# Optimization experiments

Hardware: AMD Instinct MI355X
Metric: run time of the kernel (lower is better)

Reference implementation:

```python
import jax, jax.numpy as jnp
import numpy as np

NUM_NODES = 100000
NUM_RELS = 200
DIM = 128
NUM_EDGES = 600000


def setup_inputs() -> dict:
    key = jax.random.key(0)
    ks = jax.random.split(key, 12)
    xav = lambda k, shp: jax.random.uniform(k, shp, jnp.float32, -1.0, 1.0) * jnp.sqrt(6.0 / (shp[0] + shp[1]))
    return {
        'edge_index': jax.random.randint(ks[0], (2, NUM_EDGES), 0, NUM_NODES),
        'edge_type': jax.random.randint(ks[1], (NUM_EDGES,), 0, NUM_RELS),
        'edge_weight': jax.random.uniform(ks[2], (NUM_EDGES,), jnp.float32),
        'node_emb': xav(ks[3], (NUM_NODES, DIM)),
        'rel_emb': xav(ks[4], (NUM_RELS, DIM)),
        'W0': xav(ks[5], (DIM, DIM)),
        'Wself0': xav(ks[6], (DIM, DIM)),
        'Wrel0': xav(ks[7], (DIM, DIM)),
        'W1': xav(ks[8], (DIM, DIM)),
        'Wself1': xav(ks[9], (DIM, DIM)),
        'Wrel1': xav(ks[10], (DIM, DIM)),
    }


def comp_sub(x_src, r):
    return x_src - r


def compgcn_conv(x, rel, edge_index, edge_type, edge_weight, W, Wself, Wrel):
    src, dst = edge_index[0], edge_index[1]
    # edge-wise gather + composition: [E, D]
    msg = comp_sub(x[src], rel[edge_type])
    msg = msg * edge_weight[:, None]
    # scatter-add aggregation to destination nodes: [N, D]
    agg = jax.ops.segment_sum(msg, dst, num_segments=x.shape[0])
    x_out = agg @ W + x @ Wself
    rel_out = rel @ Wrel
    return x_out, rel_out


def reference(edge_index, edge_type, edge_weight, node_emb, rel_emb,
              W0, Wself0, Wrel0, W1, Wself1, Wrel1):
    # layer 0
    x, rel = compgcn_conv(node_emb, rel_emb, edge_index, edge_type, edge_weight,
                          W0, Wself0, Wrel0)
    # inter-layer nonlinearity (dropout is identity in eval mode)
    x = jax.nn.relu(x)
    rel = jax.nn.relu(rel)
    # layer 1 (last layer: no relu/dropout after)
    x, rel = compgcn_conv(x, rel, edge_index, edge_type, edge_weight,
                          W1, Wself1, Wrel1)
    return x, rel
```

## Files before the change

### kernel.cpp

```cpp
#include <hip/hip_runtime.h>

#define DD 128
#define CAP 64

typedef __attribute__((ext_vector_type(8))) short bf16x8;
typedef __attribute__((ext_vector_type(4))) float f32x4;

__device__ __forceinline__ float b2f(unsigned short u) {
    return __uint_as_float(((unsigned)u) << 16);
}
__device__ __forceinline__ unsigned short f2b(float f) {
    unsigned u = __float_as_uint(f);
    unsigned r = (u + 0x7FFFu + ((u >> 16) & 1u)) >> 16;
    return (unsigned short)r;
}


__global__ __launch_bounds__(256) void init_kernel(int4* __restrict__ cnt4, int n4,
                                                   uint2* __restrict__ csre, int n) {
    int i = blockIdx.x * 256 + threadIdx.x;
    if (i < n4) { cnt4[i] = make_int4(0, 0, 0, 0); return; }
    i -= n4;
    if (i < n) csre[(size_t)i * CAP] = make_uint2(0u, 0u);
}


__global__ __launch_bounds__(256) void fill_conv_kernel(
    const int* __restrict__ ei, const int* __restrict__ ety,
    const float* __restrict__ ew, int* __restrict__ cnt,
    uint2* __restrict__ csre, int E, int ebl,
    const float* __restrict__ x0, unsigned short* __restrict__ xb, int bx, int n4x,
    const float* __restrict__ r0, unsigned short* __restrict__ r0b, int br, int n4r,
    const float* __restrict__ W0, const float* __restrict__ Ws0,
    const float* __restrict__ W1, const float* __restrict__ Ws1,
    const float* __restrict__ Wr0, const float* __restrict__ Wr1,
    unsigned short* __restrict__ wt0a, unsigned short* __restrict__ wt0s,
    unsigned short* __restrict__ wt1a, unsigned short* __restrict__ wt1s,
    unsigned short* __restrict__ wtr0, unsigned short* __restrict__ wtr1) {
    int bid = blockIdx.x;
    if (bid < ebl) {
        int e = bid * 256 + threadIdx.x;
        if (e < E) {
            int dst = ei[E + e];
            int pos = atomicAdd(&cnt[dst], 1);
            if (pos < CAP) {
                uint2 rec;
                rec.x = ((unsigned)ei[e]) | (((unsigned)ety[e]) << 20);
                rec.y = __float_as_uint(ew[e]);
                csre[(size_t)dst * CAP + pos] = rec;
            }
        }
        return;
    }
    bid -= ebl;
    if (bid < bx) {
        int i = bid * 256 + threadIdx.x;
        if (i < n4x) {
            float4 v = ((const float4*)x0)[i];
            ((ushort4*)xb)[i] = make_ushort4(f2b(v.x), f2b(v.y), f2b(v.z), f2b(v.w));
        }
        return;
    }
    bid -= bx;
    if (bid < br) {
        int i = bid * 256 + threadIdx.x;
        if (i < n4r) {
            float4 v = ((const float4*)r0)[i];
            ((ushort4*)r0b)[i] = make_ushort4(f2b(v.x), f2b(v.y), f2b(v.z), f2b(v.w));
        }
        return;
    }
    bid -= br;
    int which = bid >> 6;
    int i = (bid & 63) * 256 + threadIdx.x;
    int cc = i >> 7, k = i & 127;
    const float* Wsel = which == 0 ? W0 : which == 1 ? Ws0 : which == 2 ? W1
                      : which == 3 ? Ws1 : which == 4 ? Wr0 : Wr1;
    unsigned short* Osel = which == 0 ? wt0a : which == 1 ? wt0s : which == 2 ? wt1a
                         : which == 3 ? wt1s : which == 4 ? wtr0 : wtr1;
    Osel[i] = f2b(Wsel[k * DD + cc]);
}


__global__ __launch_bounds__(256) void aggregate_kernel(
    const unsigned short* __restrict__ xb, const unsigned short* __restrict__ relb,
    const int* __restrict__ cnt, const uint2* __restrict__ csre,
    unsigned short* __restrict__ aggb, int n) {
    int slot = threadIdx.x >> 4;
    int c = threadIdx.x & 15;
    int n0 = blockIdx.x * 32 + slot;
    int n1 = n0 + 16;
    int b0 = 0, e0 = 0, b1 = 0, e1 = 0;
    if (n0 < n) { b0 = n0 * CAP; e0 = b0 + min(cnt[n0], CAP); }
    if (n1 < n) { b1 = n1 * CAP; e1 = b1 + min(cnt[n1], CAP); }
    int i0 = b0, i1 = b1;
    const bf16x8* X = (const bf16x8*)xb;
    const bf16x8* Rl = (const bf16x8*)relb;
    float p0[8], q0[8], p1[8], q1[8];
#pragma unroll
    for (int j = 0; j < 8; ++j) { p0[j] = 0.f; q0[j] = 0.f; p1[j] = 0.f; q1[j] = 0.f; }
    while (i0 < e0 || i1 < e1) {
        bool v00 = i0 < e0, v01 = i0 + 1 < e0;
        bool v10 = i1 < e1, v11 = i1 + 1 < e1;
        uint2 c00 = csre[v00 ? i0 : b0];
        uint2 c01 = csre[v01 ? i0 + 1 : b0];
        uint2 c10 = csre[v10 ? i1 : b1];
        uint2 c11 = csre[v11 ? i1 + 1 : b1];
        float w00 = v00 ? __uint_as_float(c00.y) : 0.f;
        float w01 = v01 ? __uint_as_float(c01.y) : 0.f;
        float w10 = v10 ? __uint_as_float(c10.y) : 0.f;
        float w11 = v11 ? __uint_as_float(c11.y) : 0.f;
        bf16x8 x00 = X[(size_t)(c00.x & 0xFFFFFu) * 16 + c];
        bf16x8 x01 = X[(size_t)(c01.x & 0xFFFFFu) * 16 + c];
        bf16x8 x10 = X[(size_t)(c10.x & 0xFFFFFu) * 16 + c];
        bf16x8 x11 = X[(size_t)(c11.x & 0xFFFFFu) * 16 + c];
        bf16x8 r00 = Rl[(c00.x >> 20) * 16 + c];
        bf16x8 r01 = Rl[(c01.x >> 20) * 16 + c];
        bf16x8 r10 = Rl[(c10.x >> 20) * 16 + c];
        bf16x8 r11 = Rl[(c11.x >> 20) * 16 + c];
#pragma unroll
        for (int j = 0; j < 8; ++j) {
            p0[j] += (b2f((unsigned short)x00[j]) - b2f((unsigned short)r00[j])) * w00;
            q0[j] += (b2f((unsigned short)x01[j]) - b2f((unsigned short)r01[j])) * w01;
            p1[j] += (b2f((unsigned short)x10[j]) - b2f((unsigned short)r10[j])) * w10;
            q1[j] += (b2f((unsigned short)x11[j]) - b2f((unsigned short)r11[j])) * w11;
        }
        i0 = min(i0 + 2, e0);
        i1 = min(i1 + 2, e1);
    }
    if (n0 < n) {
        bf16x8 ov;
#pragma unroll
        for (int j = 0; j < 8; ++j) ov[j] = (short)f2b(p0[j] + q0[j]);
        ((bf16x8*)aggb)[(size_t)n0 * 16 + c] = ov;
    }
    if (n1 < n) {
        bf16x8 ov;
#pragma unroll
        for (int j = 0; j < 8; ++j) ov[j] = (short)f2b(p1[j] + q1[j]);
        ((bf16x8*)aggb)[(size_t)n1 * 16 + c] = ov;
    }
}


__global__ __launch_bounds__(512, 4) void mfma_dual_gemm_kernel(
    const unsigned short* __restrict__ A, const unsigned short* __restrict__ X,
    const unsigned short* __restrict__ WtA, const unsigned short* __restrict__ WtX,
    float* __restrict__ outf, unsigned short* __restrict__ outb,
    int nrows, int relu,
    const unsigned short* __restrict__ relsrc, const unsigned short* __restrict__ WtR,
    float* __restrict__ reloutf, unsigned short* __restrict__ reloutb,
    int R, int gbl) {
    __shared__ unsigned short sW[2][DD * DD];
    bool isrel = (int)blockIdx.x >= gbl;
    const unsigned short* srcA = isrel ? WtR : WtA;
    for (int i = threadIdx.x; i < 2048; i += 512) {
        int row = i >> 4, slot = i & 15;
        int so = (slot ^ (row & 15)) * 8;
        *(float4*)&sW[0][row * DD + so] = ((const float4*)srcA)[i];
        *(float4*)&sW[1][row * DD + so] = ((const float4*)WtX)[i];
    }
    __syncthreads();
    int w = threadIdx.x >> 6, l = threadIdx.x & 63;
    int lr = l & 15, lk = l >> 4;

    f32x4 acc[8];
#pragma unroll
    for (int ct = 0; ct < 8; ++ct) acc[ct] = (f32x4){0.f, 0.f, 0.f, 0.f};

    if (!isrel) {
        int row = blockIdx.x * 128 + w * 16 + lr;
        bool v = row < nrows;
#pragma unroll
        for (int kb = 0; kb < 4; ++kb) {
            int koff = kb * 32 + lk * 8;
            bf16x8 a = {}, x = {};
            if (v) {
                a = *(const bf16x8*)(A + (size_t)row * DD + koff);
                x = *(const bf16x8*)(X + (size_t)row * DD + koff);
            }
#pragma unroll
            for (int ct = 0; ct < 8; ++ct) {
                int wrow = ct * 16 + lr;
                int slot = kb * 4 + lk;
                int so = (slot ^ (wrow & 15)) * 8;
                bf16x8 bw = *(const bf16x8*)&sW[0][wrow * DD + so];
                bf16x8 bs = *(const bf16x8*)&sW[1][wrow * DD + so];
                acc[ct] = __builtin_amdgcn_mfma_f32_16x16x32_bf16(bw, a, acc[ct], 0, 0, 0);
                acc[ct] = __builtin_amdgcn_mfma_f32_16x16x32_bf16(bs, x, acc[ct], 0, 0, 0);
            }
        }
        if (v) {
#pragma unroll
            for (int ct = 0; ct < 8; ++ct) {
                f32x4 vv = acc[ct];
                if (relu) {
                    vv[0] = fmaxf(vv[0], 0.f); vv[1] = fmaxf(vv[1], 0.f);
                    vv[2] = fmaxf(vv[2], 0.f); vv[3] = fmaxf(vv[3], 0.f);
                }
                int cb = ct * 16 + lk * 4;
                if (outf) *(f32x4*)(outf + (size_t)row * DD + cb) = vv;
                if (outb) {
                    *(ushort4*)(outb + (size_t)row * DD + cb) =
                        make_ushort4(f2b(vv[0]), f2b(vv[1]), f2b(vv[2]), f2b(vv[3]));
                }
            }
        }
    } else {
        int row = ((int)blockIdx.x - gbl) * 128 + w * 16 + lr;
        bool v = row < R;
#pragma unroll
        for (int kb = 0; kb < 4; ++kb) {
            int koff = kb * 32 + lk * 8;
            bf16x8 a = {};
            if (v) a = *(const bf16x8*)(relsrc + (size_t)row * DD + koff);
#pragma unroll
            for (int ct = 0; ct < 8; ++ct) {
                int wrow = ct * 16 + lr;
                int slot = kb * 4 + lk;
                int so = (slot ^ (wrow & 15)) * 8;
                bf16x8 bw = *(const bf16x8*)&sW[0][wrow * DD + so];
                acc[ct] = __builtin_amdgcn_mfma_f32_16x16x32_bf16(bw, a, acc[ct], 0, 0, 0);
            }
        }
        if (v) {
#pragma unroll
            for (int ct = 0; ct < 8; ++ct) {
                f32x4 vv = acc[ct];
                if (relu) {
                    vv[0] = fmaxf(vv[0], 0.f); vv[1] = fmaxf(vv[1], 0.f);
                    vv[2] = fmaxf(vv[2], 0.f); vv[3] = fmaxf(vv[3], 0.f);
                }
                int cb = ct * 16 + lk * 4;
                if (reloutf) *(f32x4*)(reloutf + (size_t)row * DD + cb) = vv;
                if (reloutb) {
                    *(ushort4*)(reloutb + (size_t)row * DD + cb) =
                        make_ushort4(f2b(vv[0]), f2b(vv[1]), f2b(vv[2]), f2b(vv[3]));
                }
            }
        }
    }
}


extern "C" void kernel_launch(void* const* d_in, const int* in_sizes, int n_in,
                              void* d_out, int out_size, void* d_ws, size_t ws_size,
                              hipStream_t stream) {
    const int*   ei  = (const int*)d_in[0];
    const int*   ety = (const int*)d_in[1];
    const float* ew  = (const float*)d_in[2];
    const float* x0  = (const float*)d_in[3];
    const float* r0  = (const float*)d_in[4];
    const float* W0  = (const float*)d_in[5];
    const float* Ws0 = (const float*)d_in[6];
    const float* Wr0 = (const float*)d_in[7];
    const float* W1  = (const float*)d_in[8];
    const float* Ws1 = (const float*)d_in[9];
    const float* Wr1 = (const float*)d_in[10];

    const int E = in_sizes[1];
    const int N = in_sizes[3] / DD;
    const int R = in_sizes[4] / DD;

    float* out_x = (float*)d_out;
    float* out_r = out_x + (size_t)N * DD;

    char* w = (char*)d_ws;
    size_t off = 0;
    auto alloc = [&](size_t bytes) {
        void* p = w + off;
        off += (bytes + 255) & ~(size_t)255;
        return p;
    };
    unsigned short* aggb  = (unsigned short*)alloc((size_t)N * DD * 2);
    unsigned short* xb    = (unsigned short*)alloc((size_t)N * DD * 2);
    unsigned short* r0b   = (unsigned short*)alloc((size_t)R * DD * 2);
    unsigned short* rel1b = (unsigned short*)alloc((size_t)R * DD * 2);
    unsigned short* wt0a  = (unsigned short*)alloc((size_t)DD * DD * 2);
    unsigned short* wt0s  = (unsigned short*)alloc((size_t)DD * DD * 2);
    unsigned short* wt1a  = (unsigned short*)alloc((size_t)DD * DD * 2);
    unsigned short* wt1s  = (unsigned short*)alloc((size_t)DD * DD * 2);
    unsigned short* wtr0  = (unsigned short*)alloc((size_t)DD * DD * 2);
    unsigned short* wtr1  = (unsigned short*)alloc((size_t)DD * DD * 2);
    int*   cnt  = (int*)alloc((size_t)N * 4);
    uint2* csre = (uint2*)alloc((size_t)N * CAP * 8);
    (void)ws_size; (void)n_in; (void)out_size;

    int ebl = (E + 255) / 256;
    int n4x = N * 32, n4r = R * 32;
    int bx = (n4x + 255) / 256, br = (n4r + 255) / 256;
    int n4c = N / 4;

    init_kernel<<<(n4c + N + 255) / 256, 256, 0, stream>>>((int4*)cnt, n4c, csre, N);

    fill_conv_kernel<<<ebl + bx + br + 384, 256, 0, stream>>>(
        ei, ety, ew, cnt, csre, E, ebl,
        x0, xb, bx, n4x, r0, r0b, br, n4r,
        W0, Ws0, W1, Ws1, Wr0, Wr1,
        wt0a, wt0s, wt1a, wt1s, wtr0, wtr1);

    int abl = (N + 31) / 32;
    int gbl = (N + 127) / 128;
    int rblk = (R + 127) / 128;

    aggregate_kernel<<<abl, 256, 0, stream>>>(xb, r0b, cnt, csre, aggb, N);
    mfma_dual_gemm_kernel<<<gbl + rblk, 512, 0, stream>>>(
        aggb, xb, wt0a, wt0s, nullptr, xb, N, 1,
        r0b, wtr0, nullptr, rel1b, R, gbl);

    aggregate_kernel<<<abl, 256, 0, stream>>>(xb, rel1b, cnt, csre, aggb, N);
    mfma_dual_gemm_kernel<<<gbl + rblk, 512, 0, stream>>>(
        aggb, xb, wt1a, wt1s, out_x, nullptr, N, 0,
        rel1b, wtr1, out_r, nullptr, R, gbl);
}
```

Baseline: 176.3 us.

## Halve per-node edge capacity, interleave edge-fill blocks, clamp gather indices

Reduces the per-destination slot capacity from 64 to 32. This halves the CSR buffer footprint and stride, and it lets the init kernel drop the per-node sentinel writes and zero only the counters. The fill kernel now spreads edge-insertion blocks evenly across the grid among the conversion blocks, so the atomic work overlaps with the bf16 conversions. The aggregate kernel clamps source and relation indices, so padded or uninitialized records stay in bounds. The risk is that nodes with more than 32 incoming edges lose edges; with 600k edges over 100k nodes that is rare but possible.

```diff
diff --git a/kernel.cpp b/kernel.cpp
--- a/kernel.cpp
+++ b/kernel.cpp
@@ -1,7 +1,7 @@
 #include <hip/hip_runtime.h>
 
 #define DD 128
-#define CAP 64
+#define CAP 32
 
 typedef __attribute__((ext_vector_type(8))) short bf16x8;
 typedef __attribute__((ext_vector_type(4))) float f32x4;
@@ -16,12 +16,9 @@
 }
 
 
-__global__ __launch_bounds__(256) void init_kernel(int4* __restrict__ cnt4, int n4,
-                                                   uint2* __restrict__ csre, int n) {
+__global__ __launch_bounds__(256) void init_kernel(int4* __restrict__ z4, int n4) {
     int i = blockIdx.x * 256 + threadIdx.x;
-    if (i < n4) { cnt4[i] = make_int4(0, 0, 0, 0); return; }
-    i -= n4;
-    if (i < n) csre[(size_t)i * CAP] = make_uint2(0u, 0u);
+    if (i < n4) z4[i] = make_int4(0, 0, 0, 0);
 }
 
 
@@ -37,9 +34,12 @@
     unsigned short* __restrict__ wt0a, unsigned short* __restrict__ wt0s,
     unsigned short* __restrict__ wt1a, unsigned short* __restrict__ wt1s,
     unsigned short* __restrict__ wtr0, unsigned short* __restrict__ wtr1) {
+    int T = gridDim.x;
     int bid = blockIdx.x;
-    if (bid < ebl) {
-        int e = bid * 256 + threadIdx.x;
+    int F0 = (int)(((long long)bid * ebl) / T);
+    int F1 = (int)(((long long)(bid + 1) * ebl) / T);
+    if (F1 > F0) {
+        int e = F0 * 256 + threadIdx.x;
         if (e < E) {
             int dst = ei[E + e];
             int pos = atomicAdd(&cnt[dst], 1);
@@ -52,27 +52,27 @@
         }
         return;
     }
-    bid -= ebl;
-    if (bid < bx) {
-        int i = bid * 256 + threadIdx.x;
+    int cid = bid - F0;
+    if (cid < bx) {
+        int i = cid * 256 + threadIdx.x;
         if (i < n4x) {
             float4 v = ((const float4*)x0)[i];
             ((ushort4*)xb)[i] = make_ushort4(f2b(v.x), f2b(v.y), f2b(v.z), f2b(v.w));
         }
         return;
     }
-    bid -= bx;
-    if (bid < br) {
-        int i = bid * 256 + threadIdx.x;
+    cid -= bx;
+    if (cid < br) {
+        int i = cid * 256 + threadIdx.x;
         if (i < n4r) {
             float4 v = ((const float4*)r0)[i];
             ((ushort4*)r0b)[i] = make_ushort4(f2b(v.x), f2b(v.y), f2b(v.z), f2b(v.w));
         }
         return;
     }
-    bid -= br;
-    int which = bid >> 6;
-    int i = (bid & 63) * 256 + threadIdx.x;
+    cid -= br;
+    int which = cid >> 6;
+    int i = (cid & 63) * 256 + threadIdx.x;
     int cc = i >> 7, k = i & 127;
     const float* Wsel = which == 0 ? W0 : which == 1 ? Ws0 : which == 2 ? W1
                       : which == 3 ? Ws1 : which == 4 ? Wr0 : Wr1;
@@ -85,7 +85,7 @@
 __global__ __launch_bounds__(256) void aggregate_kernel(
     const unsigned short* __restrict__ xb, const unsigned short* __restrict__ relb,
     const int* __restrict__ cnt, const uint2* __restrict__ csre,
-    unsigned short* __restrict__ aggb, int n) {
+    unsigned short* __restrict__ aggb, int n, int R) {
     int slot = threadIdx.x >> 4;
     int c = threadIdx.x & 15;
     int n0 = blockIdx.x * 32 + slot;
@@ -110,14 +110,22 @@
         float w01 = v01 ? __uint_as_float(c01.y) : 0.f;
         float w10 = v10 ? __uint_as_float(c10.y) : 0.f;
         float w11 = v11 ? __uint_as_float(c11.y) : 0.f;
-        bf16x8 x00 = X[(size_t)(c00.x & 0xFFFFFu) * 16 + c];
-        bf16x8 x01 = X[(size_t)(c01.x & 0xFFFFFu) * 16 + c];
-        bf16x8 x10 = X[(size_t)(c10.x & 0xFFFFFu) * 16 + c];
-        bf16x8 x11 = X[(size_t)(c11.x & 0xFFFFFu) * 16 + c];
-        bf16x8 r00 = Rl[(c00.x >> 20) * 16 + c];
-        bf16x8 r01 = Rl[(c01.x >> 20) * 16 + c];
-        bf16x8 r10 = Rl[(c10.x >> 20) * 16 + c];
-        bf16x8 r11 = Rl[(c11.x >> 20) * 16 + c];
+        int s00 = min((int)(c00.x & 0xFFFFFu), n - 1);
+        int s01 = min((int)(c01.x & 0xFFFFFu), n - 1);
+        int s10 = min((int)(c10.x & 0xFFFFFu), n - 1);
+        int s11 = min((int)(c11.x & 0xFFFFFu), n - 1);
+        int t00 = min((int)(c00.x >> 20), R - 1);
+        int t01 = min((int)(c01.x >> 20), R - 1);
+        int t10 = min((int)(c10.x >> 20), R - 1);
+        int t11 = min((int)(c11.x >> 20), R - 1);
+        bf16x8 x00 = X[(size_t)s00 * 16 + c];
+        bf16x8 x01 = X[(size_t)s01 * 16 + c];
+        bf16x8 x10 = X[(size_t)s10 * 16 + c];
+        bf16x8 x11 = X[(size_t)s11 * 16 + c];
+        bf16x8 r00 = Rl[t00 * 16 + c];
+        bf16x8 r01 = Rl[t01 * 16 + c];
+        bf16x8 r10 = Rl[t10 * 16 + c];
+        bf16x8 r11 = Rl[t11 * 16 + c];
 #pragma unroll
         for (int j = 0; j < 8; ++j) {
             p0[j] += (b2f((unsigned short)x00[j]) - b2f((unsigned short)r00[j])) * w00;
@@ -289,9 +297,9 @@
     int ebl = (E + 255) / 256;
     int n4x = N * 32, n4r = R * 32;
     int bx = (n4x + 255) / 256, br = (n4r + 255) / 256;
-    int n4c = N / 4;
-
-    init_kernel<<<(n4c + N + 255) / 256, 256, 0, stream>>>((int4*)cnt, n4c, csre, N);
+    int n4z = N / 4;
+
+    init_kernel<<<(n4z + 255) / 256, 256, 0, stream>>>((int4*)cnt, n4z);
 
     fill_conv_kernel<<<ebl + bx + br + 384, 256, 0, stream>>>(
         ei, ety, ew, cnt, csre, E, ebl,
@@ -303,12 +311,12 @@
     int gbl = (N + 127) / 128;
     int rblk = (R + 127) / 128;
 
-    aggregate_kernel<<<abl, 256, 0, stream>>>(xb, r0b, cnt, csre, aggb, N);
+    aggregate_kernel<<<abl, 256, 0, stream>>>(xb, r0b, cnt, csre, aggb, N, R);
     mfma_dual_gemm_kernel<<<gbl + rblk, 512, 0, stream>>>(
         aggb, xb, wt0a, wt0s, nullptr, xb, N, 1,
         r0b, wtr0, nullptr, rel1b, R, gbl);
 
-    aggregate_kernel<<<abl, 256, 0, stream>>>(xb, rel1b, cnt, csre, aggb, N);
+    aggregate_kernel<<<abl, 256, 0, stream>>>(xb, rel1b, cnt, csre, aggb, N, R);
     mfma_dual_gemm_kernel<<<gbl + rblk, 512, 0, stream>>>(
         aggb, xb, wt1a, wt1s, out_x, nullptr, N, 0,
         rel1b, wtr1, out_r, nullptr, R, gbl);
```

Measured after the change: 184.7 us. 4.8% more time.
